# Kernel tuning notes

Measured on AMD Instinct MI355X. Metric: run time of the kernel, lower is better.

Reference implementation:

```python
import jax, jax.numpy as jnp
import numpy as np

NUM_HEADS = 16
HIDDEN = 1024
B, S = 2, 2048


def setup_inputs() -> dict:
    key = jax.random.key(0)
    ks = jax.random.split(key, 14)
    D = HIDDEN
    scale = 1.0 / np.sqrt(D)
    inp = {
        "query": jax.random.normal(ks[0], (B, S, D), jnp.float32),
        "key_in": jax.random.normal(ks[1], (B, S, D), jnp.float32),
        "value": jax.random.normal(ks[2], (B, S, D), jnp.float32),
        "group_prob": jax.random.uniform(ks[3], (B, S, S), jnp.float32),
        "mask": jax.random.randint(ks[4], (B, S, S), 0, 2, jnp.int32),
        "wq_k": jax.random.normal(ks[5], (D, D), jnp.float32) * scale,
        "wq_b": jnp.zeros((D,), jnp.float32),
        "wk_k": jax.random.normal(ks[6], (D, D), jnp.float32) * scale,
        "wk_b": jnp.zeros((D,), jnp.float32),
        "wv_k": jax.random.normal(ks[7], (D, D), jnp.float32) * scale,
        "wv_b": jnp.zeros((D,), jnp.float32),
        "wo_k": jax.random.normal(ks[8], (D, D), jnp.float32) * scale,
        "wo_b": jnp.zeros((D,), jnp.float32),
    }
    return inp


def _split_heads(x, H):
    b, s, d = x.shape
    return x.reshape(b, s, H, d // H).transpose(0, 2, 1, 3)  # (B,H,S,dh)


def reference(query, key_in, value, group_prob, mask,
              wq_k, wq_b, wk_k, wk_b, wv_k, wv_b, wo_k, wo_b):
    H = NUM_HEADS
    dh = query.shape[-1] // H
    q = _split_heads(query @ wq_k + wq_b, H)
    k = _split_heads(key_in @ wk_k + wk_b, H)
    v = _split_heads(value @ wv_k + wv_b, H)
    # scaled dot-product logits (B,H,Sq,Sk)
    logits = jnp.einsum('bhqd,bhkd->bhqk', q, k) / jnp.sqrt(jnp.asarray(dh, q.dtype))
    neg = (1.0 - mask.astype(q.dtype)) * -1e9
    logits = logits + neg[:, None, :, :]
    attn = jax.nn.softmax(logits, axis=-1)
    # Tree Transformer modulation: post-softmax elementwise scale by group_prob
    attn = attn * group_prob[:, None, :, :]
    out = jnp.einsum('bhqk,bhkd->bhqd', attn, v)
    out = out.transpose(0, 2, 1, 3).reshape(query.shape[0], -1, H * dh)
    return out @ wo_k + wo_b
```

## Files before the change

kernel.cpp:

```cpp
#include <hip/hip_runtime.h>
#include <hip/hip_bf16.h>
#include <stdint.h>

#define B_ 2
#define S_ 2048
#define D_ 1024
#define H_ 16
#define DH 64

typedef __attribute__((ext_vector_type(4))) float f32x4;
typedef __attribute__((ext_vector_type(8))) short s16x8;
typedef __attribute__((ext_vector_type(4))) short s16x4;

__device__ inline short f2bf(float f) {
  union { float f; unsigned u; } v; v.f = f;
  unsigned r = (v.u + 0x7fffu + ((v.u >> 16) & 1u)) >> 16;
  return (short)r;
}

__device__ inline float bfbits_lo(unsigned u) {
  union { unsigned x; float f; } v; v.x = u << 16; return v.f;
}
__device__ inline float bfbits_hi(unsigned u) {
  union { unsigned x; float f; } v; v.x = u & 0xffff0000u; return v.f;
}

__device__ inline float exp2v(float x) {
  float r; asm("v_exp_f32 %0, %1" : "=v"(r) : "v"(x)); return r;
}
__device__ inline unsigned cvtpk(float a, float b) {
  unsigned r; asm("v_cvt_pk_bf16_f32 %0, %1, %2" : "=v"(r) : "v"(a), "v"(b));
  return r;
}

__global__ __launch_bounds__(256) void cvt3_f32_bf16(const float* __restrict__ a,
                                                     const float* __restrict__ b,
                                                     const float* __restrict__ c,
                                                     short* oa, short* ob, short* oc,
                                                     int n) {
  int z = blockIdx.y;
  const float* in = z == 0 ? a : (z == 1 ? b : c);
  short* out = z == 0 ? oa : (z == 1 ? ob : oc);
  int i = (blockIdx.x * 256 + threadIdx.x) * 4;
  if (i < n) {
    float4 v = *(const float4*)(in + i);
    s16x4 o;
    o.x = f2bf(v.x); o.y = f2bf(v.y); o.z = f2bf(v.z); o.w = f2bf(v.w);
    *(s16x4*)(out + i) = o;
  }
}

__global__ __launch_bounds__(256) void fuse_mgp(const int* __restrict__ mask,
                                                const float* __restrict__ gp,
                                                short* __restrict__ mgp, int n) {
  int i = (blockIdx.x * 256 + threadIdx.x) * 4;
  if (i < n) {
    int4 m = *(const int4*)(mask + i);
    float4 g = *(const float4*)(gp + i);
    short b0 = f2bf(g.x); if (!b0) b0 = (short)0x0080;
    short b1 = f2bf(g.y); if (!b1) b1 = (short)0x0080;
    short b2 = f2bf(g.z); if (!b2) b2 = (short)0x0080;
    short b3 = f2bf(g.w); if (!b3) b3 = (short)0x0080;
    s16x4 o;
    o.x = m.x ? b0 : 0;
    o.y = m.y ? b1 : 0;
    o.z = m.z ? b2 : 0;
    o.w = m.w ? b3 : 0;
    *(s16x4*)(mgp + i) = o;
  }
}

__global__ __launch_bounds__(256) void transpose_cvt4(
    const float* __restrict__ i0, const float* __restrict__ i1,
    const float* __restrict__ i2, const float* __restrict__ i3,
    short* o0, short* o1, short* o2, short* o3) {
  int z = blockIdx.z;
  const float* in = z == 0 ? i0 : (z == 1 ? i1 : (z == 2 ? i2 : i3));
  short* out = z == 0 ? o0 : (z == 1 ? o1 : (z == 2 ? o2 : o3));
  __shared__ float tile[32][33];
  int bx = blockIdx.x, by = blockIdx.y;
  int x = bx * 32 + threadIdx.x;
#pragma unroll
  for (int i = 0; i < 32; i += 8) {
    int y = by * 32 + threadIdx.y + i;
    tile[threadIdx.y + i][threadIdx.x] = in[(size_t)y * D_ + x];
  }
  __syncthreads();
  int ox = by * 32 + threadIdx.x;
#pragma unroll
  for (int i = 0; i < 32; i += 8) {
    int oy = bx * 32 + threadIdx.y + i;
    out[(size_t)oy * D_ + ox] = f2bf(tile[threadIdx.x][threadIdx.y + i]);
  }
}

__global__ __launch_bounds__(256) void transpose_v(const short* __restrict__ vp,
                                                   short* __restrict__ vt) {
  __shared__ __align__(16) short t[64 * 72];
  int tid = threadIdx.x;
  int bh = blockIdx.y, b = bh >> 4, h = bh & 15;
  int s0 = blockIdx.x * 64;
  int r = tid >> 2, cc = tid & 3;
  const short* src = vp + ((size_t)(b * S_ + s0 + r)) * D_ + h * DH + cc * 16;
  s16x8 a = *(const s16x8*)src;
  s16x8 bb = *(const s16x8*)(src + 8);
  int pc = (cc ^ (r >> 4)) * 16;
  *(s16x8*)&t[r * 72 + pc] = a;
  *(s16x8*)&t[r * 72 + pc + 8] = bb;
  __syncthreads();
  int d = tid >> 2, sc = (tid & 3) * 16;
  s16x8 o0, o1;
#pragma unroll
  for (int j = 0; j < 8; ++j) {
    int row = sc + j;
    o0[j] = t[row * 72 + ((d >> 4) ^ (row >> 4)) * 16 + (d & 15)];
    int row2 = sc + 8 + j;
    o1[j] = t[row2 * 72 + ((d >> 4) ^ (row2 >> 4)) * 16 + (d & 15)];
  }
  short* dst = vt + ((size_t)(b * H_ + h) * DH + d) * S_ + s0 + sc;
  *(s16x8*)dst = o0;
  *(s16x8*)(dst + 8) = o1;
}

__device__ inline void gload_lds16(const void* g, void* l) {
  __builtin_amdgcn_global_load_lds(
      (const __attribute__((address_space(1))) unsigned*)g,
      (__attribute__((address_space(3))) unsigned*)l, 16, 0, 0);
}

#define BM 128
#define BN 128
#define BK 64

__global__ __launch_bounds__(256) void gemm_bt3(
    const short* __restrict__ A0, const short* __restrict__ A1, const short* __restrict__ A2,
    const short* __restrict__ Bt0, const short* __restrict__ Bt1, const short* __restrict__ Bt2,
    const float* __restrict__ bs0, const float* __restrict__ bs1, const float* __restrict__ bs2,
    void* C0, void* C1, void* C2,
    int M, int N, int K, int f32out, float os0, float os1, float os2) {
  int z = blockIdx.y;
  const short* A = z == 0 ? A0 : (z == 1 ? A1 : A2);
  const short* Bt = z == 0 ? Bt0 : (z == 1 ? Bt1 : Bt2);
  const float* bias = z == 0 ? bs0 : (z == 1 ? bs1 : bs2);
  void* C = z == 0 ? C0 : (z == 1 ? C1 : C2);
  float oscale = z == 0 ? os0 : (z == 1 ? os1 : os2);

  __shared__ __align__(16) short As[BM * BK];
  __shared__ __align__(16) short Bs[BN * BK];
  int tid = threadIdx.x;
  int lane = tid & 63, wave = tid >> 6;
  int l15 = lane & 15, l4 = lane >> 4;
  int ntn = N / BN;
  int bm = blockIdx.x / ntn, bn = blockIdx.x % ntn;
  int row0 = bm * BM, col0 = bn * BN;
  int wm = (wave >> 1) * 64, wn = (wave & 1) * 64;

  f32x4 acc[4][4] = {};

  for (int k0 = 0; k0 < K; k0 += BK) {
    __syncthreads();
#pragma unroll
    for (int it = 0; it < 4; ++it) {
      int ch = it * 256 + tid;
      int r = ch >> 3, c = (ch & 7) * 8;
      int ldsbase = (it * 256 + wave * 64) * 8;
      gload_lds16(A + (size_t)(row0 + r) * K + k0 + c, &As[ldsbase]);
      gload_lds16(Bt + (size_t)(col0 + r) * K + k0 + c, &Bs[ldsbase]);
    }
    __syncthreads();
#pragma unroll
    for (int ks = 0; ks < 2; ++ks) {
      s16x8 af[4], bf[4];
#pragma unroll
      for (int mf = 0; mf < 4; ++mf)
        af[mf] = *(const s16x8*)&As[(wm + mf * 16 + l15) * BK + ks * 32 + l4 * 8];
#pragma unroll
      for (int nf = 0; nf < 4; ++nf)
        bf[nf] = *(const s16x8*)&Bs[(wn + nf * 16 + l15) * BK + ks * 32 + l4 * 8];
#pragma unroll
      for (int mf = 0; mf < 4; ++mf)
#pragma unroll
        for (int nf = 0; nf < 4; ++nf)
          acc[mf][nf] = __builtin_amdgcn_mfma_f32_16x16x32_bf16(af[mf], bf[nf],
                                                                acc[mf][nf], 0, 0, 0);
    }
  }

#pragma unroll
  for (int nf = 0; nf < 4; ++nf) {
    int gcol = col0 + wn + nf * 16 + l15;
    float bv = bias[gcol];
#pragma unroll
    for (int mf = 0; mf < 4; ++mf) {
#pragma unroll
      for (int r = 0; r < 4; ++r) {
        int grow = row0 + wm + mf * 16 + l4 * 4 + r;
        float v = (acc[mf][nf][r] + bv) * oscale;
        if (f32out)
          ((float*)C)[(size_t)grow * N + gcol] = v;
        else
          ((short*)C)[(size_t)grow * N + gcol] = f2bf(v);
      }
    }
  }
}

#define QB 128
#define NB 64
#define NTILES (S_ / NB)
#define M0_SHIFT 12.0f

__global__ __launch_bounds__(256) void attn_fused(const short* __restrict__ Qp,
                                                  const short* __restrict__ Kp,
                                                  const short* __restrict__ VT,
                                                  const short* __restrict__ MGP,
                                                  short* __restrict__ ctx) {
  __shared__ __align__(16) short Ks[2][64 * 64];
  __shared__ __align__(16) short Ms[2][QB * 64];
  __shared__ __align__(16) short Vs[2][64 * 64];

  int tid = threadIdx.x, lane = tid & 63, wave = tid >> 6;
  int l15 = lane & 15, l4 = lane >> 4;
  int q0 = blockIdx.x * QB;
  int bh = blockIdx.y;
  int b = bh >> 4, h = bh & 15;
  int wq = wave * 32;

  const short* Qbase = Qp + (size_t)b * S_ * D_ + (size_t)h * DH;
  const short* Kbase = Kp + (size_t)b * S_ * D_ + (size_t)h * DH;
  const short* Vbase = VT + (size_t)(b * H_ + h) * DH * S_;
  const short* Mbase = MGP + (size_t)b * S_ * S_ + (size_t)q0 * S_;

  int i0 = tid, i1 = 256 + tid;
  int r0 = i0 >> 3, c0 = (i0 & 7) ^ (r0 & 7);
  int r1 = i1 >> 3, c1 = (i1 & 7) ^ (r1 & 7);
  int ldsA = wave * 512;
  int ldsB = 2048 + wave * 512;
  int mr[4], mc[4], mlds[4];
#pragma unroll
  for (int it = 0; it < 4; ++it) {
    int ch = it * 256 + tid;
    mr[it] = ch >> 3;
    mc[it] = (ch & 7) ^ (mr[it] & 7);
    mlds[it] = (it * 256 + wave * 64) * 8;
  }

#define STAGE(kv0, buf)                                                       \
  do {                                                                        \
    gload_lds16(Kbase + (size_t)((kv0) + r0) * D_ + c0 * 8, &Ks[buf][ldsA]);  \
    gload_lds16(Kbase + (size_t)((kv0) + r1) * D_ + c1 * 8, &Ks[buf][ldsB]);  \
    gload_lds16(Vbase + (size_t)r0 * S_ + (kv0) + c0 * 8, &Vs[buf][ldsA]);    \
    gload_lds16(Vbase + (size_t)r1 * S_ + (kv0) + c1 * 8, &Vs[buf][ldsB]);    \
    gload_lds16(Mbase + (size_t)mr[0] * S_ + (kv0) + mc[0] * 8, &Ms[buf][mlds[0]]); \
    gload_lds16(Mbase + (size_t)mr[1] * S_ + (kv0) + mc[1] * 8, &Ms[buf][mlds[1]]); \
    gload_lds16(Mbase + (size_t)mr[2] * S_ + (kv0) + mc[2] * 8, &Ms[buf][mlds[2]]); \
    gload_lds16(Mbase + (size_t)mr[3] * S_ + (kv0) + mc[3] * 8, &Ms[buf][mlds[3]]); \
  } while (0)

  s16x8 qf[2][2];
#pragma unroll
  for (int mf = 0; mf < 2; ++mf)
#pragma unroll
    for (int ks = 0; ks < 2; ++ks)
      qf[mf][ks] = *(const s16x8*)(Qbase + (size_t)(q0 + wq + mf * 16 + l15) * D_ +
                                   ks * 32 + l4 * 8);

  float lsum[2] = {0.f, 0.f};
  f32x4 oacc[2][4] = {};

  STAGE(0, 0);

  int q7 = l15 & 7;
  int q7l = q7 << 1;
  int rowoff[2] = {(wq + l15) * 64, (wq + 16 + l15) * 64};

  for (int t = 0; t < NTILES; ++t) {
    int buf = t & 1;

    if (t + 1 < NTILES) {
      STAGE((t + 1) * NB, buf ^ 1);
      asm volatile("s_waitcnt vmcnt(8)" ::: "memory");
    } else {
      asm volatile("s_waitcnt vmcnt(0)" ::: "memory");
    }
    __builtin_amdgcn_s_barrier();
    __builtin_amdgcn_sched_barrier(0);

    f32x4 sacc[2][4] = {};
#pragma unroll
    for (int nf = 0; nf < 4; ++nf) {
      int R = nf * 16 + l15;
#pragma unroll
      for (int ks = 0; ks < 2; ++ks) {
        s16x8 kf = *(const s16x8*)&Ks[buf][R * 64 + (((ks * 4 + l4) ^ q7) * 8)];
#pragma unroll
        for (int mf = 0; mf < 2; ++mf)
          sacc[mf][nf] = __builtin_amdgcn_mfma_f32_16x16x32_bf16(kf, qf[mf][ks],
                                                                 sacc[mf][nf], 0, 0, 0);
      }
    }

#pragma unroll
    for (int mf = 0; mf < 2; ++mf) {
#pragma unroll
      for (int nf = 0; nf < 4; ++nf) {
        int sl = ((nf * 4 + l4) ^ q7l) * 4;
        uint2 g2 = *(const uint2*)&Ms[buf][rowoff[mf] + sl];
        float gv0 = bfbits_lo(g2.x), gv1 = bfbits_hi(g2.x);
        float gv2 = bfbits_lo(g2.y), gv3 = bfbits_hi(g2.y);
        float e0 = exp2v(sacc[mf][nf][0] - M0_SHIFT);
        float e1 = exp2v(sacc[mf][nf][1] - M0_SHIFT);
        float e2 = exp2v(sacc[mf][nf][2] - M0_SHIFT);
        float e3 = exp2v(sacc[mf][nf][3] - M0_SHIFT);
        lsum[mf] += (gv0 != 0.f) ? e0 : 0.f;
        lsum[mf] += (gv1 != 0.f) ? e1 : 0.f;
        lsum[mf] += (gv2 != 0.f) ? e2 : 0.f;
        lsum[mf] += (gv3 != 0.f) ? e3 : 0.f;
        uint2 wp;
        wp.x = cvtpk(e0 * gv0, e1 * gv1);
        wp.y = cvtpk(e2 * gv2, e3 * gv3);
        *(uint2*)&Ms[buf][rowoff[mf] + sl] = wp;
      }
    }

#pragma unroll
    for (int ks = 0; ks < 2; ++ks) {
      s16x8 pa[2];
#pragma unroll
      for (int mf = 0; mf < 2; ++mf)
        pa[mf] = *(const s16x8*)&Ms[buf][rowoff[mf] + (((ks * 4 + l4) ^ q7) * 8)];
#pragma unroll
      for (int df = 0; df < 4; ++df) {
        s16x8 vf = *(const s16x8*)&Vs[buf][(df * 16 + l15) * 64 +
                                           (((ks * 4 + l4) ^ q7) * 8)];
#pragma unroll
        for (int mf = 0; mf < 2; ++mf)
          oacc[mf][df] = __builtin_amdgcn_mfma_f32_16x16x32_bf16(vf, pa[mf],
                                                                 oacc[mf][df], 0, 0, 0);
      }
    }

    asm volatile("s_waitcnt lgkmcnt(0)" ::: "memory");
    __builtin_amdgcn_s_barrier();
  }
#undef STAGE

#pragma unroll
  for (int mf = 0; mf < 2; ++mf) {
    float ls = lsum[mf];
    ls += __shfl_xor(ls, 16);
    ls += __shfl_xor(ls, 32);
    float inv = 1.f / ls;
    short* crow = ctx + ((size_t)(b * S_ + q0 + wq + mf * 16 + l15)) * D_ + h * DH;
#pragma unroll
    for (int df = 0; df < 4; ++df) {
      uint2 o;
      o.x = cvtpk(oacc[mf][df][0] * inv, oacc[mf][df][1] * inv);
      o.y = cvtpk(oacc[mf][df][2] * inv, oacc[mf][df][3] * inv);
      *(uint2*)(crow + df * 16 + l4 * 4) = o;
    }
  }
}

extern "C" void kernel_launch(void* const* d_in, const int* in_sizes, int n_in,
                              void* d_out, int out_size, void* d_ws, size_t ws_size,
                              hipStream_t stream) {
  const float* query = (const float*)d_in[0];
  const float* key_in = (const float*)d_in[1];
  const float* value = (const float*)d_in[2];
  const float* group_prob = (const float*)d_in[3];
  const int* mask = (const int*)d_in[4];
  const float* wq_k = (const float*)d_in[5];
  const float* wq_b = (const float*)d_in[6];
  const float* wk_k = (const float*)d_in[7];
  const float* wk_b = (const float*)d_in[8];
  const float* wv_k = (const float*)d_in[9];
  const float* wv_b = (const float*)d_in[10];
  const float* wo_k = (const float*)d_in[11];
  const float* wo_b = (const float*)d_in[12];
  float* out = (float*)d_out;

  short* ws = (short*)d_ws;
  const size_t NT = (size_t)B_ * S_ * D_;
  short* qbf = ws;
  short* kbf = qbf + NT;
  short* vbf = kbf + NT;
  short* wqt = vbf + NT;
  short* wkt = wqt + (size_t)D_ * D_;
  short* wvt = wkt + (size_t)D_ * D_;
  short* wot = wvt + (size_t)D_ * D_;
  short* qp = wot + (size_t)D_ * D_;
  short* kp = qp + NT;
  short* vp = kp + NT;
  short* ctx = vp + NT;
  short* mgp = ws;
  short* vt = vbf;

  int nblk = (int)(NT / 4 / 256);
  cvt3_f32_bf16<<<dim3(nblk, 3), 256, 0, stream>>>(query, key_in, value,
                                                   qbf, kbf, vbf, (int)NT);

  dim3 tb(32, 8);
  transpose_cvt4<<<dim3(D_ / 32, D_ / 32, 4), tb, 0, stream>>>(
      wq_k, wk_k, wv_k, wo_k, wqt, wkt, wvt, wot);

  int M = B_ * S_;
  int gblocks = (M / BM) * (D_ / BN);
  const float QSCALE = 0.125f * 1.4426950408889634f;
  gemm_bt3<<<dim3(gblocks, 3), 256, 0, stream>>>(
      qbf, kbf, vbf, wqt, wkt, wvt, wq_b, wk_b, wv_b, qp, kp, vp,
      M, D_, D_, 0, QSCALE, 1.0f, 1.0f);

  int nmg = B_ * S_ * S_;
  fuse_mgp<<<nmg / 4 / 256, 256, 0, stream>>>(mask, group_prob, mgp, nmg);
  transpose_v<<<dim3(S_ / 64, B_ * H_), 256, 0, stream>>>(vp, vt);

  dim3 ag(S_ / QB, B_ * H_);
  attn_fused<<<ag, 256, 0, stream>>>(qp, kp, vt, mgp, ctx);

  gemm_bt3<<<dim3(gblocks, 1), 256, 0, stream>>>(
      ctx, ctx, ctx, wot, wot, wot, wo_b, wo_b, wo_b, out, out, out,
      M, D_, D_, 1, 1.0f, 1.0f, 1.0f);
}
```

Before: 195.2 us.

## Load mask/group-prob directly to registers and shrink attention LDS footprint

The attention kernel no longer stages the combined mask/group-prob tile through double-buffered LDS. Each lane now loads its own fragment straight into registers, with waitcnt values retuned so these loads overlap the QK MFMAs. P is written to a smaller per-wave LDS scratch, which cuts LDS use and adds a 3-blocks-per-SM launch bound to raise occupancy. Separately, the QKV GEMM K-tile is halved to 32, trading fewer LDS bytes per stage for more barriers per K loop.

```diff
diff --git a/kernel.cpp b/kernel.cpp
--- a/kernel.cpp
+++ b/kernel.cpp
@@ -130,7 +130,7 @@
 
 #define BM 128
 #define BN 128
-#define BK 64
+#define BK 32
 
 __global__ __launch_bounds__(256) void gemm_bt3(
     const short* __restrict__ A0, const short* __restrict__ A1, const short* __restrict__ A2,
@@ -160,30 +160,27 @@
   for (int k0 = 0; k0 < K; k0 += BK) {
     __syncthreads();
 #pragma unroll
-    for (int it = 0; it < 4; ++it) {
+    for (int it = 0; it < 2; ++it) {
       int ch = it * 256 + tid;
-      int r = ch >> 3, c = (ch & 7) * 8;
+      int r = ch >> 2, c = (ch & 3) * 8;
       int ldsbase = (it * 256 + wave * 64) * 8;
       gload_lds16(A + (size_t)(row0 + r) * K + k0 + c, &As[ldsbase]);
       gload_lds16(Bt + (size_t)(col0 + r) * K + k0 + c, &Bs[ldsbase]);
     }
     __syncthreads();
-#pragma unroll
-    for (int ks = 0; ks < 2; ++ks) {
-      s16x8 af[4], bf[4];
-#pragma unroll
-      for (int mf = 0; mf < 4; ++mf)
-        af[mf] = *(const s16x8*)&As[(wm + mf * 16 + l15) * BK + ks * 32 + l4 * 8];
+    s16x8 af[4], bf[4];
+#pragma unroll
+    for (int mf = 0; mf < 4; ++mf)
+      af[mf] = *(const s16x8*)&As[(wm + mf * 16 + l15) * BK + l4 * 8];
+#pragma unroll
+    for (int nf = 0; nf < 4; ++nf)
+      bf[nf] = *(const s16x8*)&Bs[(wn + nf * 16 + l15) * BK + l4 * 8];
+#pragma unroll
+    for (int mf = 0; mf < 4; ++mf)
 #pragma unroll
       for (int nf = 0; nf < 4; ++nf)
-        bf[nf] = *(const s16x8*)&Bs[(wn + nf * 16 + l15) * BK + ks * 32 + l4 * 8];
-#pragma unroll
-      for (int mf = 0; mf < 4; ++mf)
-#pragma unroll
-        for (int nf = 0; nf < 4; ++nf)
-          acc[mf][nf] = __builtin_amdgcn_mfma_f32_16x16x32_bf16(af[mf], bf[nf],
-                                                                acc[mf][nf], 0, 0, 0);
-    }
+        acc[mf][nf] = __builtin_amdgcn_mfma_f32_16x16x32_bf16(af[mf], bf[nf],
+                                                              acc[mf][nf], 0, 0, 0);
   }
 
 #pragma unroll
@@ -210,14 +207,14 @@
 #define NTILES (S_ / NB)
 #define M0_SHIFT 12.0f
 
-__global__ __launch_bounds__(256) void attn_fused(const short* __restrict__ Qp,
-                                                  const short* __restrict__ Kp,
-                                                  const short* __restrict__ VT,
-                                                  const short* __restrict__ MGP,
-                                                  short* __restrict__ ctx) {
+__global__ __launch_bounds__(256, 3) void attn_fused(const short* __restrict__ Qp,
+                                                     const short* __restrict__ Kp,
+                                                     const short* __restrict__ VT,
+                                                     const short* __restrict__ MGP,
+                                                     short* __restrict__ ctx) {
   __shared__ __align__(16) short Ks[2][64 * 64];
-  __shared__ __align__(16) short Ms[2][QB * 64];
   __shared__ __align__(16) short Vs[2][64 * 64];
+  __shared__ __align__(16) short Ps[4][32 * 64];
 
   int tid = threadIdx.x, lane = tid & 63, wave = tid >> 6;
   int l15 = lane & 15, l4 = lane >> 4;
@@ -229,21 +226,14 @@
   const short* Qbase = Qp + (size_t)b * S_ * D_ + (size_t)h * DH;
   const short* Kbase = Kp + (size_t)b * S_ * D_ + (size_t)h * DH;
   const short* Vbase = VT + (size_t)(b * H_ + h) * DH * S_;
-  const short* Mbase = MGP + (size_t)b * S_ * S_ + (size_t)q0 * S_;
+  const short* Mrow0 = MGP + (size_t)b * S_ * S_ + (size_t)(q0 + wq + l15) * S_ + l4 * 4;
+  const short* Mrow1 = Mrow0 + (size_t)16 * S_;
 
   int i0 = tid, i1 = 256 + tid;
   int r0 = i0 >> 3, c0 = (i0 & 7) ^ (r0 & 7);
   int r1 = i1 >> 3, c1 = (i1 & 7) ^ (r1 & 7);
   int ldsA = wave * 512;
   int ldsB = 2048 + wave * 512;
-  int mr[4], mc[4], mlds[4];
-#pragma unroll
-  for (int it = 0; it < 4; ++it) {
-    int ch = it * 256 + tid;
-    mr[it] = ch >> 3;
-    mc[it] = (ch & 7) ^ (mr[it] & 7);
-    mlds[it] = (it * 256 + wave * 64) * 8;
-  }
 
 #define STAGE(kv0, buf)                                                       \
   do {                                                                        \
@@ -251,10 +241,6 @@
     gload_lds16(Kbase + (size_t)((kv0) + r1) * D_ + c1 * 8, &Ks[buf][ldsB]);  \
     gload_lds16(Vbase + (size_t)r0 * S_ + (kv0) + c0 * 8, &Vs[buf][ldsA]);    \
     gload_lds16(Vbase + (size_t)r1 * S_ + (kv0) + c1 * 8, &Vs[buf][ldsB]);    \
-    gload_lds16(Mbase + (size_t)mr[0] * S_ + (kv0) + mc[0] * 8, &Ms[buf][mlds[0]]); \
-    gload_lds16(Mbase + (size_t)mr[1] * S_ + (kv0) + mc[1] * 8, &Ms[buf][mlds[1]]); \
-    gload_lds16(Mbase + (size_t)mr[2] * S_ + (kv0) + mc[2] * 8, &Ms[buf][mlds[2]]); \
-    gload_lds16(Mbase + (size_t)mr[3] * S_ + (kv0) + mc[3] * 8, &Ms[buf][mlds[3]]); \
   } while (0)
 
   s16x8 qf[2][2];
@@ -271,17 +257,27 @@
   STAGE(0, 0);
 
   int q7 = l15 & 7;
-  int q7l = q7 << 1;
-  int rowoff[2] = {(wq + l15) * 64, (wq + 16 + l15) * 64};
+  short* Pw = &Ps[wave][0];
+  int prow[2] = {l15 * 64, (16 + l15) * 64};
 
   for (int t = 0; t < NTILES; ++t) {
     int buf = t & 1;
-
+    int kvt = t * NB;
+
+    uint2 g2[2][4];
+#pragma unroll
+    for (int nf = 0; nf < 4; ++nf) {
+      g2[0][nf] = *(const uint2*)(Mrow0 + kvt + nf * 16);
+      g2[1][nf] = *(const uint2*)(Mrow1 + kvt + nf * 16);
+    }
+    __builtin_amdgcn_sched_barrier(0);
     if (t + 1 < NTILES) {
       STAGE((t + 1) * NB, buf ^ 1);
+      __builtin_amdgcn_sched_barrier(0);
+      asm volatile("s_waitcnt vmcnt(12)" ::: "memory");
+    } else {
+      __builtin_amdgcn_sched_barrier(0);
       asm volatile("s_waitcnt vmcnt(8)" ::: "memory");
-    } else {
-      asm volatile("s_waitcnt vmcnt(0)" ::: "memory");
     }
     __builtin_amdgcn_s_barrier();
     __builtin_amdgcn_sched_barrier(0);
@@ -300,14 +296,18 @@
       }
     }
 
+    if (t + 1 < NTILES)
+      asm volatile("s_waitcnt vmcnt(4)" ::: "memory");
+    else
+      asm volatile("s_waitcnt vmcnt(0)" ::: "memory");
+    __builtin_amdgcn_sched_barrier(0);
+
 #pragma unroll
     for (int mf = 0; mf < 2; ++mf) {
 #pragma unroll
       for (int nf = 0; nf < 4; ++nf) {
-        int sl = ((nf * 4 + l4) ^ q7l) * 4;
-        uint2 g2 = *(const uint2*)&Ms[buf][rowoff[mf] + sl];
-        float gv0 = bfbits_lo(g2.x), gv1 = bfbits_hi(g2.x);
-        float gv2 = bfbits_lo(g2.y), gv3 = bfbits_hi(g2.y);
+        float gv0 = bfbits_lo(g2[mf][nf].x), gv1 = bfbits_hi(g2[mf][nf].x);
+        float gv2 = bfbits_lo(g2[mf][nf].y), gv3 = bfbits_hi(g2[mf][nf].y);
         float e0 = exp2v(sacc[mf][nf][0] - M0_SHIFT);
         float e1 = exp2v(sacc[mf][nf][1] - M0_SHIFT);
         float e2 = exp2v(sacc[mf][nf][2] - M0_SHIFT);
@@ -319,7 +319,8 @@
         uint2 wp;
         wp.x = cvtpk(e0 * gv0, e1 * gv1);
         wp.y = cvtpk(e2 * gv2, e3 * gv3);
-        *(uint2*)&Ms[buf][rowoff[mf] + sl] = wp;
+        int gr = ((nf * 2 + (l4 >> 1)) ^ q7) * 8 + (l4 & 1) * 4;
+        *(uint2*)&Pw[prow[mf] + gr] = wp;
       }
     }
 
@@ -328,7 +329,7 @@
       s16x8 pa[2];
 #pragma unroll
       for (int mf = 0; mf < 2; ++mf)
-        pa[mf] = *(const s16x8*)&Ms[buf][rowoff[mf] + (((ks * 4 + l4) ^ q7) * 8)];
+        pa[mf] = *(const s16x8*)&Pw[prow[mf] + (((ks * 4 + l4) ^ q7) * 8)];
 #pragma unroll
       for (int df = 0; df < 4; ++df) {
         s16x8 vf = *(const s16x8*)&Vs[buf][(df * 16 + l15) * 64 +
```

After: 188.0 us. 1.04x faster.
